# Kernel optimization log

Hardware: AMD Instinct MI355X
Metric: run time of the kernel (lower is better)

## Reference

```python
import jax, jax.numpy as jnp
import numpy as np

B, F, V, D = 16384, 16, 100000, 16  # batch, n_fields, vocab, embed_dim; dims = F*D = 256
EPS = 1e-5


def _bn(x, g, b):
    # torch.nn.BatchNorm1d in training mode: biased batch variance
    m = x.mean(0)
    v = x.var(0)
    return g * (x - m) * jax.lax.rsqrt(v + EPS) + b


def setup_inputs() -> dict:
    ks = iter(jax.random.split(jax.random.key(0), 40))

    def rn(shape, s=0.05):
        return jax.random.normal(next(ks), shape, jnp.float32) * s

    return {
        "feat_ids": jax.random.randint(next(ks), (B, F), 0, V, jnp.int32),
        "domain_ids": jax.random.randint(next(ks), (B,), 0, 3, jnp.int32),
        "emb": rn((F, V, D), 0.1),
        "hW0": rn((256, 128)), "hb0": jnp.zeros(128), "hg0": jnp.ones(128), "hbe0": jnp.zeros(128),
        "hW1": rn((128, 64)), "hb1": jnp.zeros(64), "hg1": jnp.ones(64), "hbe1": jnp.zeros(64),
        "hW2": rn((64, 1024)), "hb2": jnp.zeros(1024), "hg2": jnp.ones(1024), "hbe2": jnp.zeros(1024),
        "cw": rn((3, 256)), "cb": jnp.zeros((3, 256)),
        "mW0": rn((256, 512)), "mb0": jnp.zeros(512), "mg0": jnp.ones(512), "mbe0": jnp.zeros(512),
        "mW1": rn((512, 256)), "mb1": jnp.zeros(256), "mg1": jnp.ones(256), "mbe1": jnp.zeros(256),
        "u0": rn((256, 32)), "u1": rn((32, 32)), "v0": rn((32, 32)), "v1": rn((32, 256)),
        "ab0": jnp.zeros(32), "ab1": jnp.zeros(256),
        "gamma1": jnp.ones(256), "bias1": jnp.zeros(256),
        "lw": rn((512,)), "lb": jnp.zeros(1),
    }


def _forward(feat_ids, emb, hW0, hb0, hg0, hbe0, hW1, hb1, hg1, hbe1,
             hW2, hb2, hg2, hbe2, cw, cb, mW0, mb0, mg0, mbe0,
             mW1, mb1, mg1, mbe1, u0, u1, v0, v1, ab0, ab1,
             gamma1, bias1, lw, lb):
    b, f = feat_ids.shape
    # EmbeddingLayer(squeeze_dim=True): per-field lookup then concat -> [B, F*D]
    e = emb[jnp.arange(f)[None, :], feat_ids].reshape(b, -1)
    h = e
    for W, bb, g, be in ((hW0, hb0, hg0, hbe0), (hW1, hb1, hg1, hbe1), (hW2, hb2, hg2, hbe2)):
        h = jax.nn.relu(_bn(h @ W + bb, g, be))
    k = u1.shape[0]
    H = h.reshape(b, k, k)  # [B, k, k]
    # CrossNetwork: x_{l+1} = x0 * (x_l . w_l) + b_l + x_l
    x = e
    for i in range(cw.shape[0]):
        x = e * (x @ cw[i])[:, None] + cb[i] + x
    cn_out = x  # [B, 256]
    m = e
    for W, bb, g, be in ((mW0, mb0, mg0, mbe0), (mW1, mb1, mg1, mbe1)):
        m = jax.nn.relu(_bn(m @ W + bb, g, be))
    # hyper low-rank adapter: einsum('mi,bij,jn->bmn') applied lazily so the
    # [B,256,32] per-sample weight is never materialized (associativity)
    t = jax.nn.sigmoid(jnp.einsum('bi,bij->bj', m @ u0, H) @ v0 + ab0)   # [B, 32]
    t = jnp.einsum('bi,bij->bj', t @ u1, H) @ v1 + ab1                    # [B, 256]
    mu = t.mean(0)
    var = t.var(0, ddof=1)  # torch.var default is unbiased
    m = gamma1 * (t - mu) / jnp.sqrt(var + EPS) + bias1 + m  # norm + residual
    y = jnp.concatenate([cn_out, m], axis=1) @ lw + lb[0]     # LR head
    # Every domain branch computes identical values (shared weights, full-batch
    # input, dropout p=0), so the torch.where domain-select is the identity.
    return jax.nn.sigmoid(y)  # [B]


def reference(feat_ids, domain_ids, emb, hW0, hb0, hg0, hbe0, hW1, hb1, hg1, hbe1,
              hW2, hb2, hg2, hbe2, cw, cb, mW0, mb0, mg0, mbe0,
              mW1, mb1, mg1, mbe1, u0, u1, v0, v1, ab0, ab1,
              gamma1, bias1, lw, lb):
    return _forward(feat_ids, emb, hW0, hb0, hg0, hbe0, hW1, hb1, hg1, hbe1,
                    hW2, hb2, hg2, hbe2, cw, cb, mW0, mb0, mg0, mbe0,
                    mW1, mb1, mg1, mbe1, u0, u1, v0, v1, ab0, ab1,
                    gamma1, bias1, lw, lb)
```

## Files before the change

kernel.cpp:

```cpp
#include <hip/hip_runtime.h>

typedef unsigned short u16;
typedef __attribute__((ext_vector_type(8))) short bf16x8;
typedef __attribute__((ext_vector_type(4))) float f32x4;
#define BATCH 16384

__device__ __forceinline__ float b2f(u16 u){ unsigned int i=((unsigned int)u)<<16; float f; __builtin_memcpy(&f,&i,4); return f; }
__device__ __forceinline__ u16 f2b(float f){ unsigned int x; __builtin_memcpy(&x,&f,4); unsigned int r=(x + 0x7fffu + ((x>>16)&1u))>>16; return (u16)r; }

__global__ __launch_bounds__(256) void prep_kernel(float* __restrict__ S,
                                                   const float* __restrict__ hb0, const float* __restrict__ mb0,
                                                   float* __restrict__ catb,
                                                   const float* __restrict__ w0, const float* __restrict__ w1,
                                                   const float* __restrict__ w2, const float* __restrict__ w3,
                                                   const float* __restrict__ w4, const float* __restrict__ w5,
                                                   const float* __restrict__ w6,
                                                   u16* __restrict__ catWt, u16* __restrict__ t1,
                                                   u16* __restrict__ t2, u16* __restrict__ t4,
                                                   u16* __restrict__ t5, u16* __restrict__ t6,
                                                   const int* __restrict__ ids,
                                                   const float* __restrict__ emb,
                                                   u16* __restrict__ e){
  int blk = blockIdx.x;
  int tid = threadIdx.x;
  if (blk < 18){
    int i = blk*256 + tid;
    if (i < 4480) S[i] = 0.f;
  } else if (blk == 18){
    for (int i = tid; i < 640; i += 256) catb[i] = (i < 128) ? hb0[i] : mb0[i-128];
  } else if (blk < 1523){
    int c = blk - 19;
    if (c < 640){        int idx=c*256+tid;        int n=idx>>8, k=idx&255;
                         catWt[idx] = f2b(n<128 ? w0[k*128+n] : w3[k*512+(n-128)]); }
    else if (c < 672){   int idx=(c-640)*256+tid;  t1[idx]=f2b(w1[(idx%128)*64   + idx/128]); }
    else if (c < 928){   int idx=(c-672)*256+tid;  t2[idx]=f2b(w2[(idx%64)*1024  + idx/64]);  }
    else if (c < 1440){  int idx=(c-928)*256+tid;  t4[idx]=f2b(w4[(idx%512)*256  + idx/512]); }
    else if (c < 1472){  int idx=(c-1440)*256+tid; t5[idx]=f2b(w5[(idx%256)*32   + idx/256]); }
    else {               int idx=(c-1472)*256+tid; t6[idx]=f2b(w6[(idx%32)*256   + idx/32]);  }
  } else {
    int g = blk - 1523;
    int b = g*16 + (tid >> 4), f = tid & 15;
    int id = ids[b*16 + f];
    const float4* src = (const float4*)(emb + ((size_t)f*100000 + (size_t)id)*16);
    float4 v0 = src[0], v1 = src[1], v2 = src[2], v3 = src[3];
    u16 o[16] = { f2b(v0.x),f2b(v0.y),f2b(v0.z),f2b(v0.w), f2b(v1.x),f2b(v1.y),f2b(v1.z),f2b(v1.w),
                  f2b(v2.x),f2b(v2.y),f2b(v2.z),f2b(v2.w), f2b(v3.x),f2b(v3.y),f2b(v3.z),f2b(v3.w) };
    uint4 p0, p1; __builtin_memcpy(&p0, &o[0], 16); __builtin_memcpy(&p1, &o[8], 16);
    uint4* dst = (uint4*)(e + (size_t)b*256 + f*16);
    dst[0] = p0; dst[1] = p1;
  }
}

template<int BK>
__device__ __forceinline__ void gemm_body(const u16* __restrict__ A,
                                          const u16* __restrict__ Wt,
                                          const float* __restrict__ bias,
                                          u16* __restrict__ Ca,
                                          u16* __restrict__ Cb,
                                          int Nsplit,
                                          const float* __restrict__ asums,
                                          const float* __restrict__ asumsq,
                                          const float* __restrict__ ag,
                                          const float* __restrict__ abe,
                                          float* __restrict__ sums,
                                          float* __restrict__ sumsq,
                                          int N, int K, int n0, int m0,
                                          u16* lds, float* bnS, float* bnB){
  constexpr int STR = BK + 8;
  constexpr int EPT = BK/4;
  u16* As = lds;
  u16* Bs = lds + 64*STR;
  int tid = threadIdx.x;
  int lane = tid & 63, w = tid >> 6, quad = lane >> 4, m16 = lane & 15;
  int srow = tid >> 2, skoff = (tid & 3)*EPT;
  if (asums != nullptr){
    for (int k = tid; k < K; k += 256){
      float mean = asums[k] * (1.f/(float)BATCH);
      float var  = asumsq[k] * (1.f/(float)BATCH) - mean*mean;
      float sc   = ag[k] * rsqrtf(var + 1e-5f);
      bnS[k] = sc;
      bnB[k] = abe[k] - mean*sc;
    }
    __syncthreads();
  }
  f32x4 acc[4] = {};
  int ng = n0 + srow;
  uint4 a0, a1, b0, b1;
  {
    const u16* ap = A + (size_t)(m0+srow)*K + skoff;
    a0 = *(const uint4*)ap;
    if (EPT == 16) a1 = *(const uint4*)(ap + 8);
    if (ng < N){
      const u16* bp = Wt + (size_t)ng*K + skoff;
      b0 = *(const uint4*)bp;
      if (EPT == 16) b1 = *(const uint4*)(bp + 8);
    } else { b0 = make_uint4(0u,0u,0u,0u); b1 = b0; }
  }
  for (int k0 = 0; k0 < K; k0 += BK){
    u16 at[EPT];
    __builtin_memcpy(at, &a0, 16);
    if (EPT == 16) __builtin_memcpy(at+8, &a1, 16);
    if (asums != nullptr){
#pragma unroll
      for (int j=0;j<EPT;j++){
        float v = b2f(at[j]) * bnS[k0+skoff+j] + bnB[k0+skoff+j];
        at[j] = f2b(v > 0.f ? v : 0.f);
      }
    }
    uint4 s0, s1;
    __builtin_memcpy(&s0, at, 16);
    *(uint4*)&As[srow*STR + skoff] = s0;
    if (EPT == 16){ __builtin_memcpy(&s1, at+8, 16); *(uint4*)&As[srow*STR + skoff + 8] = s1; }
    *(uint4*)&Bs[srow*STR + skoff] = b0;
    if (EPT == 16) *(uint4*)&Bs[srow*STR + skoff + 8] = b1;
    if (k0 + BK < K){
      const u16* ap = A + (size_t)(m0+srow)*K + k0 + BK + skoff;
      a0 = *(const uint4*)ap;
      if (EPT == 16) a1 = *(const uint4*)(ap + 8);
      if (ng < N){
        const u16* bp = Wt + (size_t)ng*K + k0 + BK + skoff;
        b0 = *(const uint4*)bp;
        if (EPT == 16) b1 = *(const uint4*)(bp + 8);
      }
    }
    __syncthreads();
#pragma unroll
    for (int sub=0; sub<BK/32; sub++){
      bf16x8 bfrag = *(bf16x8*)&Bs[(w*16 + m16)*STR + sub*32 + quad*8];
#pragma unroll
      for (int mc=0;mc<4;mc++){
        bf16x8 afrag = *(bf16x8*)&As[(mc*16 + m16)*STR + sub*32 + quad*8];
        acc[mc] = __builtin_amdgcn_mfma_f32_16x16x32_bf16(afrag, bfrag, acc[mc], 0, 0, 0);
      }
    }
    __syncthreads();
  }
  int cw = n0 + w*16 + m16;
  float bvv = (bias != nullptr && cw < N) ? bias[cw] : 0.f;
  float cs = 0.f, cq = 0.f;
  u16* Cs = lds;
#pragma unroll
  for (int mc=0;mc<4;mc++)
#pragma unroll
    for (int r=0;r<4;r++){
      float v = acc[mc][r] + bvv;
      cs += v; cq += v*v;
      Cs[(mc*16 + quad*4 + r)*72 + w*16 + m16] = f2b(v);
    }
  if (sums != nullptr){
    cs += __shfl_xor(cs, 16, 64); cs += __shfl_xor(cs, 32, 64);
    cq += __shfl_xor(cq, 16, 64); cq += __shfl_xor(cq, 32, 64);
    if (quad == 0 && cw < N){ atomicAdd(&sums[cw], cs); atomicAdd(&sumsq[cw], cq); }
  }
  __syncthreads();
  int row = tid >> 2, c4 = (tid & 3)*16;
  int cg = n0 + c4;
  if (cg < N){
    u16* outp; int stride, colbase;
    if (Cb != nullptr && n0 >= Nsplit){ outp = Cb; stride = N - Nsplit; colbase = cg - Nsplit; }
    else if (Cb != nullptr){            outp = Ca; stride = Nsplit;     colbase = cg; }
    else {                              outp = Ca; stride = N;          colbase = cg; }
    uint4 p0 = *(uint4*)&Cs[row*72 + c4];
    uint4 p1 = *(uint4*)&Cs[row*72 + c4 + 8];
    *(uint4*)(outp + (size_t)(m0+row)*stride + colbase) = p0;
    *(uint4*)(outp + (size_t)(m0+row)*stride + colbase + 8) = p1;
  }
}

template<int BK>
__global__ __launch_bounds__(256) void gemm_mfma(const u16* __restrict__ A,
                                                 const u16* __restrict__ Wt,
                                                 const float* __restrict__ bias,
                                                 u16* __restrict__ Ca,
                                                 u16* __restrict__ Cb,
                                                 int Nsplit,
                                                 const float* __restrict__ asums,
                                                 const float* __restrict__ asumsq,
                                                 const float* __restrict__ ag,
                                                 const float* __restrict__ abe,
                                                 float* __restrict__ sums,
                                                 float* __restrict__ sumsq,
                                                 int N, int K){
  constexpr int STR = BK + 8;
  __shared__ __align__(16) u16 lds[64*STR*2];
  __shared__ float bnS[512], bnB[512];
  gemm_body<BK>(A, Wt, bias, Ca, Cb, Nsplit, asums, asumsq, ag, abe,
                sums, sumsq, N, K, blockIdx.x*64, blockIdx.y*64, lds, bnS, bnB);
}

__global__ __launch_bounds__(256) void gemm_dual(
    const u16* __restrict__ A1, const u16* __restrict__ Wt1, const float* __restrict__ b1,
    u16* __restrict__ C1,
    const float* __restrict__ as1, const float* __restrict__ aq1,
    const float* __restrict__ g1v, const float* __restrict__ be1,
    float* __restrict__ s1, float* __restrict__ q1, int N1, int K1, int nb1, int nblk1,
    const u16* __restrict__ A2, const u16* __restrict__ Wt2, const float* __restrict__ b2,
    u16* __restrict__ C2,
    const float* __restrict__ as2, const float* __restrict__ aq2,
    const float* __restrict__ g2v, const float* __restrict__ be2,
    float* __restrict__ s2, float* __restrict__ q2, int N2, int K2, int nblk2){
  constexpr int STR = 64 + 8;
  __shared__ __align__(16) u16 lds[64*STR*2];
  __shared__ float bnS[512], bnB[512];
  int blk = blockIdx.x;
  if (blk < nb1){
    int n0 = (blk % nblk1)*64, m0 = (blk / nblk1)*64;
    gemm_body<64>(A1, Wt1, b1, C1, nullptr, 0, as1, aq1, g1v, be1,
                  s1, q1, N1, K1, n0, m0, lds, bnS, bnB);
  } else {
    int q = blk - nb1;
    int n0 = (q % nblk2)*64, m0 = (q / nblk2)*64;
    gemm_body<64>(A2, Wt2, b2, C2, nullptr, 0, as2, aq2, g2v, be2,
                  s2, q2, N2, K2, n0, m0, lds, bnS, bnB);
  }
}

__global__ __launch_bounds__(256) void tables_kernel(const float* __restrict__ hsums,
                                                     const float* __restrict__ hsumsq,
                                                     const float* __restrict__ hg,
                                                     const float* __restrict__ hbe,
                                                     const float* __restrict__ msums,
                                                     const float* __restrict__ msumsq,
                                                     const float* __restrict__ mg,
                                                     const float* __restrict__ mbe,
                                                     float* __restrict__ hSg,
                                                     float* __restrict__ hBg,
                                                     float* __restrict__ mSg,
                                                     float* __restrict__ mBg){
  int i = blockIdx.x*256 + threadIdx.x;
  if (i < 1024){
    float mean = hsums[i] * (1.f/(float)BATCH);
    float var  = hsumsq[i] * (1.f/(float)BATCH) - mean*mean;
    float sc   = hg[i] * rsqrtf(var + 1e-5f);
    hSg[i] = sc; hBg[i] = hbe[i] - mean*sc;
    if (i < 256){
      float mmean = msums[i] * (1.f/(float)BATCH);
      float mvar  = msumsq[i] * (1.f/(float)BATCH) - mmean*mmean;
      float msc   = mg[i] * rsqrtf(mvar + 1e-5f);
      mSg[i] = msc; mBg[i] = mbe[i] - mmean*msc;
    }
  }
}

#define HSTR 1056
__global__ __launch_bounds__(512) void adapter_core(const u16* __restrict__ H,
                                                    const u16* __restrict__ Mout,
                                                    const u16* __restrict__ u0t,
                                                    const float* __restrict__ v0,
                                                    const float* __restrict__ u1,
                                                    const float* __restrict__ ab0,
                                                    const float* __restrict__ hSg,
                                                    const float* __restrict__ hBg,
                                                    const float* __restrict__ mSg,
                                                    const float* __restrict__ mBg,
                                                    u16* __restrict__ Z2){
  __shared__ __align__(16) u16 Hs[16*HSTR];
  __shared__ __align__(8) u16 v0s[1024], u1s[1024];
  __shared__ float PT[512], QS[512];
  __shared__ float ab0s[32];
  int tid = threadIdx.x;
  int r = tid >> 5, j = tid & 31;
  size_t row0 = (size_t)blockIdx.x * 16;
  u16* aS = Hs;

  const u16* Hb = H + row0*1024 + tid*8;
  uint4 h0 = *(const uint4*)(Hb);
  uint4 h1 = *(const uint4*)(Hb + 4096);
  uint4 h2 = *(const uint4*)(Hb + 8192);
  uint4 h3 = *(const uint4*)(Hb + 12288);

  {
    int el = tid*8, col = el & 255;
    uint4 mv = *(const uint4*)(Mout + row0*256 + el);
    float4 s0 = *(const float4*)(mSg + col), s1 = *(const float4*)(mSg + col + 4);
    float4 bb0 = *(const float4*)(mBg + col), bb1 = *(const float4*)(mBg + col + 4);
    float sv[8] = { s0.x,s0.y,s0.z,s0.w, s1.x,s1.y,s1.z,s1.w };
    float bv[8] = { bb0.x,bb0.y,bb0.z,bb0.w, bb1.x,bb1.y,bb1.z,bb1.w };
    u16 mt[8]; __builtin_memcpy(mt, &mv, 16);
#pragma unroll
    for (int q=0;q<8;q++){
      float v = b2f(mt[q]) * sv[q] + bv[q];
      mt[q] = f2b(v > 0.f ? v : 0.f);
    }
    uint4 so; __builtin_memcpy(&so, mt, 16);
    *(uint4*)&aS[el] = so;
  }
  if (tid < 256){
    float4 a = *(const float4*)(v0 + tid*4);
    ushort4 pa = { f2b(a.x), f2b(a.y), f2b(a.z), f2b(a.w) };
    *(ushort4*)&v0s[tid*4] = pa;
    float4 b4 = *(const float4*)(u1 + tid*4);
    ushort4 pb = { f2b(b4.x), f2b(b4.y), f2b(b4.z), f2b(b4.w) };
    *(ushort4*)&u1s[tid*4] = pb;
  } else if (tid < 288){
    ab0s[tid-256] = ab0[tid-256];
  }

  {
    float acc = 0.f;
    for (int k8 = 0; k8 < 256; k8 += 8){
      uint4 vu = *(const uint4*)(u0t + j*256 + k8);
      uint4 va; __builtin_memcpy(&va, &aS[r*256 + k8], 16);
      u16 ta[8], tu[8]; __builtin_memcpy(ta, &va, 16); __builtin_memcpy(tu, &vu, 16);
#pragma unroll
      for (int q=0;q<8;q++) acc += b2f(ta[q]) * b2f(tu[q]);
    }
    PT[tid] = acc;
  }
  __syncthreads();

#pragma unroll
  for (int it=0; it<4; it++){
    int el = it*4096 + tid*8;
    int rr = el >> 10, col = el & 1023;
    uint4 hv = (it==0)?h0:(it==1)?h1:(it==2)?h2:h3;
    float4 s0 = *(const float4*)(hSg + col), s1 = *(const float4*)(hSg + col + 4);
    float4 bb0 = *(const float4*)(hBg + col), bb1 = *(const float4*)(hBg + col + 4);
    float sv[8] = { s0.x,s0.y,s0.z,s0.w, s1.x,s1.y,s1.z,s1.w };
    float bv[8] = { bb0.x,bb0.y,bb0.z,bb0.w, bb1.x,bb1.y,bb1.z,bb1.w };
    u16 ht[8]; __builtin_memcpy(ht, &hv, 16);
#pragma unroll
    for (int q=0;q<8;q++){
      float v = b2f(ht[q]) * sv[q] + bv[q];
      ht[q] = f2b(v > 0.f ? v : 0.f);
    }
    uint4 so; __builtin_memcpy(&so, ht, 16);
    *(uint4*)&Hs[rr*HSTR + col] = so;
  }
  __syncthreads();

  float acc = 0.f;
#pragma unroll
  for (int i=0;i<32;i++) acc += PT[r*32+i] * b2f(Hs[r*HSTR + i*32 + j]);
  QS[tid] = acc;
  acc = ab0s[j];
#pragma unroll
  for (int i=0;i<32;i++) acc += QS[r*32+i] * b2f(v0s[i*32+j]);
  PT[tid] = 1.f / (1.f + __expf(-acc));
  acc = 0.f;
#pragma unroll
  for (int i=0;i<32;i++) acc += PT[r*32+i] * b2f(u1s[i*32+j]);
  QS[tid] = acc;
  acc = 0.f;
#pragma unroll
  for (int i=0;i<32;i++) acc += QS[r*32+i] * b2f(Hs[r*HSTR + i*32 + j]);
  Z2[(row0 + r)*32 + j] = f2b(acc);
}

__global__ __launch_bounds__(256) void final_kernel(const u16* __restrict__ e,
                                                    const float* __restrict__ cw,
                                                    const float* __restrict__ cb,
                                                    const u16* __restrict__ t,
                                                    const u16* __restrict__ mo,
                                                    const float* __restrict__ tsums,
                                                    const float* __restrict__ tsumsq,
                                                    const float* __restrict__ tg,
                                                    const float* __restrict__ tbe,
                                                    const float* __restrict__ mSg,
                                                    const float* __restrict__ mBg,
                                                    const float* __restrict__ lw,
                                                    const float* __restrict__ lb,
                                                    float* __restrict__ out){
  __shared__ float tS[256], tB[256], mS[256], mB[256];
  int tid = threadIdx.x;
  {
    int c = tid;
    float mean = tsums[c] * (1.f/(float)BATCH);
    float var  = (tsumsq[c] - mean*mean*(float)BATCH) * (1.f/(float)(BATCH-1));
    float sc   = tg[c] * rsqrtf(var + 1e-5f);
    tS[c] = sc; tB[c] = tbe[c] - mean*sc;
    mS[c] = mSg[c]; mB[c] = mBg[c];
  }
  __syncthreads();
  int wave = tid >> 6, lane = tid & 63;
  int b = blockIdx.x*4 + wave;
  int n4 = lane*4;
  ushort4 ev = *(const ushort4*)(e + (size_t)b*256 + n4);
  float ec[4] = { b2f(ev.x), b2f(ev.y), b2f(ev.z), b2f(ev.w) };
  float x[4]  = { ec[0], ec[1], ec[2], ec[3] };
  for (int i=0;i<3;i++){
    float p = 0.f;
#pragma unroll
    for (int q=0;q<4;q++) p += x[q] * cw[i*256 + n4 + q];
#pragma unroll
    for (int o=1;o<64;o<<=1) p += __shfl_xor(p, o, 64);
#pragma unroll
    for (int q=0;q<4;q++) x[q] = ec[q]*p + cb[i*256 + n4 + q] + x[q];
  }
  ushort4 tv = *(const ushort4*)(t  + (size_t)b*256 + n4);
  ushort4 mv = *(const ushort4*)(mo + (size_t)b*256 + n4);
  float ta[4] = { b2f(tv.x), b2f(tv.y), b2f(tv.z), b2f(tv.w) };
  float ma[4] = { b2f(mv.x), b2f(mv.y), b2f(mv.z), b2f(mv.w) };
  float p = 0.f;
#pragma unroll
  for (int q=0;q<4;q++){
    int n = n4 + q;
    p += x[q] * lw[n];
    float mr = ma[q]*mS[n] + mB[n];
    mr = mr > 0.f ? mr : 0.f;
    float mf = tS[n]*ta[q] + tB[n] + mr;
    p += mf * lw[256 + n];
  }
#pragma unroll
  for (int o=32;o>0;o>>=1) p += __shfl_down(p, o, 64);
  if (lane == 0){
    float y = p + lb[0];
    out[b] = 1.f / (1.f + __expf(-y));
  }
}

extern "C" void kernel_launch(void* const* d_in, const int* in_sizes, int n_in,
                              void* d_out, int out_size, void* d_ws, size_t ws_size,
                              hipStream_t stream) {
  const int B = BATCH;
  const int*   feat = (const int*)d_in[0];
  const float* emb  = (const float*)d_in[2];
  const float* hW0 = (const float*)d_in[3],  *hb0 = (const float*)d_in[4],  *hg0 = (const float*)d_in[5],  *hbe0 = (const float*)d_in[6];
  const float* hW1 = (const float*)d_in[7],  *hb1 = (const float*)d_in[8],  *hg1 = (const float*)d_in[9],  *hbe1 = (const float*)d_in[10];
  const float* hW2 = (const float*)d_in[11], *hb2 = (const float*)d_in[12], *hg2 = (const float*)d_in[13], *hbe2 = (const float*)d_in[14];
  const float* cw  = (const float*)d_in[15], *cb  = (const float*)d_in[16];
  const float* mW0 = (const float*)d_in[17], *mb0 = (const float*)d_in[18], *mg0 = (const float*)d_in[19], *mbe0 = (const float*)d_in[20];
  const float* mW1 = (const float*)d_in[21], *mb1 = (const float*)d_in[22], *mg1 = (const float*)d_in[23], *mbe1 = (const float*)d_in[24];
  const float* u0  = (const float*)d_in[25], *u1  = (const float*)d_in[26];
  const float* v0  = (const float*)d_in[27], *v1  = (const float*)d_in[28];
  const float* ab0 = (const float*)d_in[29], *ab1 = (const float*)d_in[30];
  const float* gamma1 = (const float*)d_in[31], *bias1 = (const float*)d_in[32];
  const float* lw  = (const float*)d_in[33], *lb = (const float*)d_in[34];
  float* out = (float*)d_out;

  char* base = (char*)d_ws;
  const size_t MB = 1024*1024;
  u16* H    = (u16*)(base);
  u16* e    = (u16*)(base + 32*MB);
  u16* Y0   = (u16*)(base + 40*MB);
  u16* Y1   = (u16*)(base + 44*MB);
  u16* M0   = (u16*)(base + 48*MB);
  u16* Mout = (u16*)(base + 64*MB);
  u16* T    = (u16*)(base + 72*MB);
  u16* Z2   = (u16*)(base + 80*MB);
  float* TZ = (float*)(base + 82*MB);
  u16* catWt= (u16*)(base + 88*MB);
  u16* hW1t = catWt + 163840;
  u16* hW2t = hW1t + 8192;
  u16* mW1t = hW2t + 65536;
  u16* u0t  = mW1t + 131072;
  u16* v1t  = u0t + 8192;
  float* catb = (float*)(v1t + 8192);
  float* S    = catb + 640;

  float* hSg = TZ;
  float* hBg = TZ + 1024;
  float* mSg = TZ + 2048;
  float* mBg = TZ + 2304;

  prep_kernel<<<2547, 256, 0, stream>>>(S, hb0, mb0, catb,
                                        hW0, hW1, hW2, mW0, mW1, u0, v1,
                                        catWt, hW1t, hW2t, mW1t, u0t, v1t,
                                        feat, emb, e);

  gemm_mfma<64><<<dim3(10, B/64), 256, 0, stream>>>(e, catWt, catb, Y0, M0, 128,
      nullptr, nullptr, nullptr, nullptr, S+0, S+640, 640, 256);

  gemm_dual<<<1280, 256, 0, stream>>>(
      Y0, hW1t, hb1, Y1, S+0, S+640, hg0, hbe0, S+1280, S+1344, 64, 128, 256, 1,
      M0, mW1t, mb1, Mout, S+128, S+768, mg0, mbe0, S+3456, S+3712, 256, 512, 4);

  gemm_mfma<64><<<dim3(16, B/64), 256, 0, stream>>>(Y1, hW2t, hb2, H, nullptr, 0,
      S+1280, S+1344, hg1, hbe1, S+1408, S+2432, 1024, 64);

  tables_kernel<<<4, 256, 0, stream>>>(S+1408, S+2432, hg2, hbe2,
                                       S+3456, S+3712, mg1, mbe1,
                                       hSg, hBg, mSg, mBg);

  adapter_core<<<B/16, 512, 0, stream>>>(H, Mout, u0t, v0, u1, ab0,
      hSg, hBg, mSg, mBg, Z2);
  gemm_mfma<32><<<dim3(4, B/64), 256, 0, stream>>>(Z2, v1t, ab1, T, nullptr, 0,
      nullptr, nullptr, nullptr, nullptr, S+3968, S+4224, 256, 32);

  final_kernel<<<B/4, 256, 0, stream>>>(e, cw, cb, T, Mout,
      S+3968, S+4224, gamma1, bias1, mSg, mBg, lw, lb, out);
}
```

Measured before the change: 327.5 us.

## Compute hyper-layer-2 BN stats via Gram matrix and recompute H inside adapter

```diff
diff --git a/kernel.cpp b/kernel.cpp
--- a/kernel.cpp
+++ b/kernel.cpp
@@ -23,13 +23,13 @@
                                                    u16* __restrict__ e){
   int blk = blockIdx.x;
   int tid = threadIdx.x;
-  if (blk < 18){
+  if (blk < 34){
     int i = blk*256 + tid;
-    if (i < 4480) S[i] = 0.f;
-  } else if (blk == 18){
+    if (i < 8640) S[i] = 0.f;
+  } else if (blk == 34){
     for (int i = tid; i < 640; i += 256) catb[i] = (i < 128) ? hb0[i] : mb0[i-128];
-  } else if (blk < 1523){
-    int c = blk - 19;
+  } else if (blk < 1539){
+    int c = blk - 35;
     if (c < 640){        int idx=c*256+tid;        int n=idx>>8, k=idx&255;
                          catWt[idx] = f2b(n<128 ? w0[k*128+n] : w3[k*512+(n-128)]); }
     else if (c < 672){   int idx=(c-640)*256+tid;  t1[idx]=f2b(w1[(idx%128)*64   + idx/128]); }
@@ -38,7 +38,7 @@
     else if (c < 1472){  int idx=(c-1440)*256+tid; t5[idx]=f2b(w5[(idx%256)*32   + idx/256]); }
     else {               int idx=(c-1472)*256+tid; t6[idx]=f2b(w6[(idx%32)*256   + idx/32]);  }
   } else {
-    int g = blk - 1523;
+    int g = blk - 1539;
     int b = g*16 + (tid >> 4), f = tid & 15;
     int id = ids[b*16 + f];
     const float4* src = (const float4*)(emb + ((size_t)f*100000 + (size_t)id)*16);
@@ -215,10 +215,60 @@
   }
 }
 
-__global__ __launch_bounds__(256) void tables_kernel(const float* __restrict__ hsums,
-                                                     const float* __restrict__ hsumsq,
-                                                     const float* __restrict__ hg,
-                                                     const float* __restrict__ hbe,
+__global__ __launch_bounds__(256) void gram_kernel(const u16* __restrict__ Y1,
+                                                   const float* __restrict__ g1sums,
+                                                   const float* __restrict__ g1sq,
+                                                   const float* __restrict__ hg1,
+                                                   const float* __restrict__ hbe1,
+                                                   float* __restrict__ gram,
+                                                   float* __restrict__ colsum){
+  __shared__ __align__(16) u16 ya[64*72];
+  __shared__ float g1S[64], g1B[64];
+  int tid = threadIdx.x;
+  int row = tid >> 2, koff = (tid & 3)*16;
+  size_t row0 = (size_t)blockIdx.x * 64;
+  const u16* yp = Y1 + (row0 + row)*64 + koff;
+  uint4 v0 = *(const uint4*)yp;
+  uint4 v1 = *(const uint4*)(yp + 8);
+  if (tid < 64){
+    float mean = g1sums[tid] * (1.f/(float)BATCH);
+    float var  = g1sq[tid] * (1.f/(float)BATCH) - mean*mean;
+    float sc   = hg1[tid] * rsqrtf(var + 1e-5f);
+    g1S[tid] = sc; g1B[tid] = hbe1[tid] - mean*sc;
+  }
+  __syncthreads();
+  u16 t[16]; __builtin_memcpy(t, &v0, 16); __builtin_memcpy(t+8, &v1, 16);
+#pragma unroll
+  for (int q=0;q<16;q++){
+    float v = b2f(t[q]) * g1S[koff+q] + g1B[koff+q];
+    t[q] = f2b(v > 0.f ? v : 0.f);
+  }
+  uint4 s0, s1; __builtin_memcpy(&s0, t, 16); __builtin_memcpy(&s1, t+8, 16);
+  *(uint4*)&ya[row*72 + koff] = s0;
+  *(uint4*)&ya[row*72 + koff + 8] = s1;
+  __syncthreads();
+  int gi = tid >> 2, jb = (tid & 3)*16;
+  float acc[16] = {};
+  for (int r=0;r<64;r++){
+    float yi = b2f(ya[r*72 + gi]);
+#pragma unroll
+    for (int jj=0;jj<16;jj++) acc[jj] += yi * b2f(ya[r*72 + jb + jj]);
+  }
+#pragma unroll
+  for (int jj=0;jj<16;jj++) atomicAdd(&gram[gi*64 + jb + jj], acc[jj]);
+  if (tid < 64){
+    float c = 0.f;
+    for (int r=0;r<64;r++) c += b2f(ya[r*72 + tid]);
+    atomicAdd(&colsum[tid], c);
+  }
+}
+
+__global__ __launch_bounds__(256) void tables_kernel(const float* __restrict__ gram,
+                                                     const float* __restrict__ colsum,
+                                                     const u16* __restrict__ hW2t,
+                                                     const float* __restrict__ hb2,
+                                                     const float* __restrict__ hg2,
+                                                     const float* __restrict__ hbe2,
                                                      const float* __restrict__ msums,
                                                      const float* __restrict__ msumsq,
                                                      const float* __restrict__ mg,
@@ -227,48 +277,90 @@
                                                      float* __restrict__ hBg,
                                                      float* __restrict__ mSg,
                                                      float* __restrict__ mBg){
-  int i = blockIdx.x*256 + threadIdx.x;
-  if (i < 1024){
-    float mean = hsums[i] * (1.f/(float)BATCH);
-    float var  = hsumsq[i] * (1.f/(float)BATCH) - mean*mean;
-    float sc   = hg[i] * rsqrtf(var + 1e-5f);
-    hSg[i] = sc; hBg[i] = hbe[i] - mean*sc;
-    if (i < 256){
-      float mmean = msums[i] * (1.f/(float)BATCH);
-      float mvar  = msumsq[i] * (1.f/(float)BATCH) - mmean*mmean;
-      float msc   = mg[i] * rsqrtf(mvar + 1e-5f);
-      mSg[i] = msc; mBg[i] = mbe[i] - mmean*msc;
-    }
+  __shared__ float Gs[4096];
+  __shared__ float cs[64];
+  int tid = threadIdx.x;
+  int i = blockIdx.x*256 + tid;
+  for (int k = tid; k < 4096; k += 256) Gs[k] = gram[k];
+  if (tid < 64) cs[tid] = colsum[tid];
+  __syncthreads();
+  float w[64];
+  {
+    const uint4* wr = (const uint4*)(hW2t + (size_t)i*64);
+    u16 tw[64];
+#pragma unroll
+    for (int q8=0;q8<8;q8++){ uint4 v = wr[q8]; __builtin_memcpy(tw + q8*8, &v, 16); }
+#pragma unroll
+    for (int k=0;k<64;k++) w[k] = b2f(tw[k]);
+  }
+  float sv = 0.f;
+#pragma unroll
+  for (int k=0;k<64;k++) sv += cs[k]*w[k];
+  float qf = 0.f;
+  for (int k=0;k<64;k++){
+    float u = 0.f;
+#pragma unroll
+    for (int jj=0;jj<64;jj++) u += Gs[k*64+jj]*w[jj];
+    qf += u*w[k];
+  }
+  float a = hb2[i];
+  float tsum = sv + (float)BATCH*a;
+  float tsq  = qf + 2.f*a*sv + (float)BATCH*a*a;
+  float mean = tsum * (1.f/(float)BATCH);
+  float var  = tsq * (1.f/(float)BATCH) - mean*mean;
+  float sc   = hg2[i] * rsqrtf(var + 1e-5f);
+  hSg[i] = sc; hBg[i] = hbe2[i] - mean*sc;
+  if (i < 256){
+    float mmean = msums[i] * (1.f/(float)BATCH);
+    float mvar  = msumsq[i] * (1.f/(float)BATCH) - mmean*mmean;
+    float msc   = mg[i] * rsqrtf(mvar + 1e-5f);
+    mSg[i] = msc; mBg[i] = mbe[i] - mmean*msc;
   }
 }
 
 #define HSTR 1056
-__global__ __launch_bounds__(512) void adapter_core(const u16* __restrict__ H,
+__global__ __launch_bounds__(512) void adapter_core(const u16* __restrict__ Y1,
                                                     const u16* __restrict__ Mout,
+                                                    const u16* __restrict__ hW2t,
+                                                    const float* __restrict__ hb2,
                                                     const u16* __restrict__ u0t,
                                                     const float* __restrict__ v0,
                                                     const float* __restrict__ u1,
                                                     const float* __restrict__ ab0,
+                                                    const float* __restrict__ g1sums,
+                                                    const float* __restrict__ g1sq,
+                                                    const float* __restrict__ hg1,
+                                                    const float* __restrict__ hbe1,
                                                     const float* __restrict__ hSg,
                                                     const float* __restrict__ hBg,
                                                     const float* __restrict__ mSg,
                                                     const float* __restrict__ mBg,
-                                                    u16* __restrict__ Z2){
+                                                    const u16* __restrict__ v1t,
+                                                    const float* __restrict__ ab1,
+                                                    u16* __restrict__ T,
+                                                    float* __restrict__ tsums,
+                                                    float* __restrict__ tsumsq){
   __shared__ __align__(16) u16 Hs[16*HSTR];
+  __shared__ __align__(16) u16 yaS[16*72];
   __shared__ __align__(8) u16 v0s[1024], u1s[1024];
   __shared__ float PT[512], QS[512];
+  __shared__ float g1S[64], g1B[64];
   __shared__ float ab0s[32];
   int tid = threadIdx.x;
   int r = tid >> 5, j = tid & 31;
+  int lane = tid & 63, w = tid >> 6, quad = lane >> 4, m16 = lane & 15;
   size_t row0 = (size_t)blockIdx.x * 16;
   u16* aS = Hs;
 
-  const u16* Hb = H + row0*1024 + tid*8;
-  uint4 h0 = *(const uint4*)(Hb);
-  uint4 h1 = *(const uint4*)(Hb + 4096);
-  uint4 h2 = *(const uint4*)(Hb + 8192);
-  uint4 h3 = *(const uint4*)(Hb + 12288);
-
+  uint4 yv;
+  if (tid < 128) yv = *(const uint4*)(Y1 + row0*64 + tid*8);
+  if (tid >= 128 && tid < 192){
+    int k = tid - 128;
+    float mean = g1sums[k] * (1.f/(float)BATCH);
+    float var  = g1sq[k] * (1.f/(float)BATCH) - mean*mean;
+    float sc   = hg1[k] * rsqrtf(var + 1e-5f);
+    g1S[k] = sc; g1B[k] = hbe1[k] - mean*sc;
+  }
   {
     int el = tid*8, col = el & 255;
     uint4 mv = *(const uint4*)(Mout + row0*256 + el);
@@ -309,23 +401,40 @@
   }
   __syncthreads();
 
-#pragma unroll
-  for (int it=0; it<4; it++){
-    int el = it*4096 + tid*8;
-    int rr = el >> 10, col = el & 1023;
-    uint4 hv = (it==0)?h0:(it==1)?h1:(it==2)?h2:h3;
-    float4 s0 = *(const float4*)(hSg + col), s1 = *(const float4*)(hSg + col + 4);
-    float4 bb0 = *(const float4*)(hBg + col), bb1 = *(const float4*)(hBg + col + 4);
-    float sv[8] = { s0.x,s0.y,s0.z,s0.w, s1.x,s1.y,s1.z,s1.w };
-    float bv[8] = { bb0.x,bb0.y,bb0.z,bb0.w, bb1.x,bb1.y,bb1.z,bb1.w };
-    u16 ht[8]; __builtin_memcpy(ht, &hv, 16);
+  if (tid < 128){
+    int yrow = tid >> 3, ycol = (tid & 7)*8;
+    u16 yt[8]; __builtin_memcpy(yt, &yv, 16);
 #pragma unroll
     for (int q=0;q<8;q++){
-      float v = b2f(ht[q]) * sv[q] + bv[q];
-      ht[q] = f2b(v > 0.f ? v : 0.f);
-    }
-    uint4 so; __builtin_memcpy(&so, ht, 16);
-    *(uint4*)&Hs[rr*HSTR + col] = so;
+      float v = b2f(yt[q]) * g1S[ycol+q] + g1B[ycol+q];
+      yt[q] = f2b(v > 0.f ? v : 0.f);
+    }
+    uint4 so; __builtin_memcpy(&so, yt, 16);
+    *(uint4*)&yaS[yrow*72 + ycol] = so;
+  }
+  __syncthreads();
+
+  {
+    bf16x8 a0 = *(const bf16x8*)&yaS[m16*72 + quad*8];
+    bf16x8 a1 = *(const bf16x8*)&yaS[m16*72 + 32 + quad*8];
+    int nbase = w*128;
+#pragma unroll
+    for (int nt=0;nt<8;nt++){
+      int nb = nbase + nt*16;
+      const u16* bp = hW2t + (size_t)(nb + m16)*64 + quad*8;
+      bf16x8 bf0 = *(const bf16x8*)bp;
+      bf16x8 bf1 = *(const bf16x8*)(bp + 32);
+      f32x4 acc = {0.f,0.f,0.f,0.f};
+      acc = __builtin_amdgcn_mfma_f32_16x16x32_bf16(a0, bf0, acc, 0, 0, 0);
+      acc = __builtin_amdgcn_mfma_f32_16x16x32_bf16(a1, bf1, acc, 0, 0, 0);
+      int c = nb + m16;
+      float bb = hb2[c], sc = hSg[c], bi = hBg[c];
+#pragma unroll
+      for (int rr=0;rr<4;rr++){
+        float v = (acc[rr] + bb)*sc + bi;
+        Hs[(quad*4 + rr)*HSTR + c] = f2b(v > 0.f ? v : 0.f);
+      }
+    }
   }
   __syncthreads();
 
@@ -344,7 +453,37 @@
   acc = 0.f;
 #pragma unroll
   for (int i=0;i<32;i++) acc += QS[r*32+i] * b2f(Hs[r*HSTR + i*32 + j]);
-  Z2[(row0 + r)*32 + j] = f2b(acc);
+  PT[tid] = b2f(f2b(acc));
+  __syncthreads();
+
+  u16* Ts = Hs;
+#pragma unroll
+  for (int c8=0;c8<8;c8++){
+    int c = j + 32*c8;
+    const u16* vp = v1t + (size_t)c*32;
+    uint4 q0 = *(const uint4*)vp, q1 = *(const uint4*)(vp+8);
+    uint4 q2 = *(const uint4*)(vp+16), q3 = *(const uint4*)(vp+24);
+    u16 tv[32];
+    __builtin_memcpy(tv, &q0, 16);    __builtin_memcpy(tv+8, &q1, 16);
+    __builtin_memcpy(tv+16, &q2, 16); __builtin_memcpy(tv+24, &q3, 16);
+    float t = ab1[c];
+#pragma unroll
+    for (int k=0;k<32;k++) t += PT[r*32+k] * b2f(tv[k]);
+    Ts[r*264 + c] = f2b(t);
+  }
+  __syncthreads();
+
+  if (tid < 256){
+    float s = 0.f, qq = 0.f;
+#pragma unroll
+    for (int rr=0;rr<16;rr++){ float v = b2f(Ts[rr*264 + tid]); s += v; qq += v*v; }
+    atomicAdd(&tsums[tid], s); atomicAdd(&tsumsq[tid], qq);
+  }
+  {
+    int rr = tid >> 5, cb = (tid & 31)*8;
+    uint4 pv = *(uint4*)&Ts[rr*264 + cb];
+    *(uint4*)(T + (row0 + rr)*256 + cb) = pv;
+  }
 }
 
 __global__ __launch_bounds__(256) void final_kernel(const u16* __restrict__ e,
@@ -430,16 +569,14 @@
 
   char* base = (char*)d_ws;
   const size_t MB = 1024*1024;
-  u16* H    = (u16*)(base);
-  u16* e    = (u16*)(base + 32*MB);
-  u16* Y0   = (u16*)(base + 40*MB);
-  u16* Y1   = (u16*)(base + 44*MB);
-  u16* M0   = (u16*)(base + 48*MB);
-  u16* Mout = (u16*)(base + 64*MB);
-  u16* T    = (u16*)(base + 72*MB);
-  u16* Z2   = (u16*)(base + 80*MB);
-  float* TZ = (float*)(base + 82*MB);
-  u16* catWt= (u16*)(base + 88*MB);
+  u16* e    = (u16*)(base);
+  u16* Y0   = (u16*)(base + 8*MB);
+  u16* Y1   = (u16*)(base + 12*MB);
+  u16* M0   = (u16*)(base + 16*MB);
+  u16* Mout = (u16*)(base + 32*MB);
+  u16* T    = (u16*)(base + 40*MB);
+  float* TZ = (float*)(base + 48*MB);
+  u16* catWt= (u16*)(base + 49*MB);
   u16* hW1t = catWt + 163840;
   u16* hW2t = hW1t + 8192;
   u16* mW1t = hW2t + 65536;
@@ -452,8 +589,10 @@
   float* hBg = TZ + 1024;
   float* mSg = TZ + 2048;
   float* mBg = TZ + 2304;
-
-  prep_kernel<<<2547, 256, 0, stream>>>(S, hb0, mb0, catb,
+  float* gram    = S + 4480;
+  float* colsum  = S + 8576;
+
+  prep_kernel<<<2563, 256, 0, stream>>>(S, hb0, mb0, catb,
                                         hW0, hW1, hW2, mW0, mW1, u0, v1,
                                         catWt, hW1t, hW2t, mW1t, u0t, v1t,
                                         feat, emb, e);
@@ -465,17 +604,15 @@
       Y0, hW1t, hb1, Y1, S+0, S+640, hg0, hbe0, S+1280, S+1344, 64, 128, 256, 1,
       M0, mW1t, mb1, Mout, S+128, S+768, mg0, mbe0, S+3456, S+3712, 256, 512, 4);
 
-  gemm_mfma<64><<<dim3(16, B/64), 256, 0, stream>>>(Y1, hW2t, hb2, H, nullptr, 0,
-      S+1280, S+1344, hg1, hbe1, S+1408, S+2432, 1024, 64);
-
-  tables_kernel<<<4, 256, 0, stream>>>(S+1408, S+2432, hg2, hbe2,
+  gram_kernel<<<B/64, 256, 0, stream>>>(Y1, S+1280, S+1344, hg1, hbe1, gram, colsum);
+
+  tables_kernel<<<4, 256, 0, stream>>>(gram, colsum, hW2t, hb2, hg2, hbe2,
                                        S+3456, S+3712, mg1, mbe1,
                                        hSg, hBg, mSg, mBg);
 
-  adapter_core<<<B/16, 512, 0, stream>>>(H, Mout, u0t, v0, u1, ab0,
-      hSg, hBg, mSg, mBg, Z2);
-  gemm_mfma<32><<<dim3(4, B/64), 256, 0, stream>>>(Z2, v1t, ab1, T, nullptr, 0,
-      nullptr, nullptr, nullptr, nullptr, S+3968, S+4224, 256, 32);
+  adapter_core<<<B/16, 512, 0, stream>>>(Y1, Mout, hW2t, hb2, u0t, v0, u1, ab0,
+      S+1280, S+1344, hg1, hbe1, hSg, hBg, mSg, mBg, v1t, ab1,
+      T, S+3968, S+4224);
 
   final_kernel<<<B/4, 256, 0, stream>>>(e, cw, cb, T, Mout,
       S+3968, S+4224, gamma1, bias1, mSg, mBg, lw, lb, out);
```

Result: slower. 539.3 us (+64.7%).
